# Optimization experiments

Hardware: AMD Instinct MI355X
Metric: run time of the kernel (lower is better)

The kernel has to match this reference:

```python
import jax, jax.numpy as jnp
import numpy as np


def setup_inputs() -> dict:
    key = jax.random.key(0)
    kA, kB = jax.random.split(key)
    N = 8192
    A = jax.random.normal(kA, (N, N), dtype=jnp.float32)
    B = jax.random.normal(kB, (N, N), dtype=jnp.float32)
    return {"A": A, "B": B}


def reference(A, B):
    # Kernel computes C[i,j] = sum_{k=i..j} A[i,k] * B[k,j] for i <= j, 0 elsewhere.
    # This equals triu(triu(A) @ triu(B)): k>=i is enforced by triu(A),
    # k<=j by triu(B), and output restricted to the upper triangle.
    C = jnp.triu(A) @ jnp.triu(B)
    return jnp.triu(C)
```

## Files before the change

kernel.cpp:

```cpp
#include <hip/hip_runtime.h>
#include <hip/hip_bf16.h>
#include <stdint.h>

static constexpr int ND = 8192;

typedef __attribute__((ext_vector_type(8))) short bf16x8;
typedef __attribute__((ext_vector_type(4))) float f32x4;

#define GLOBAL_AS __attribute__((address_space(1)))
#define LDS_AS __attribute__((address_space(3)))

__device__ __forceinline__ void gld_lds16(const void* g, void* l) {
    __builtin_amdgcn_global_load_lds((const GLOBAL_AS void*)g, (LDS_AS void*)l, 16, 0, 0);
}

__device__ __forceinline__ unsigned short f2bf(float x) {
    union { float f; uint32_t u; } v; v.f = x;
    uint32_t u = v.u;
    uint32_t r = (u + 0x7fffu + ((u >> 16) & 1u)) >> 16;
    return (unsigned short)r;
}

__global__ void conv_a(const float* __restrict__ A, unsigned short* __restrict__ Aw) {
    uint32_t g = blockIdx.x * 256u + threadIdx.x;
    int i  = (int)(g >> 10);
    int k0 = (int)(g & 1023u) << 3;
    if (k0 + 8 <= (i & ~255)) return;
    const float* src = A + (size_t)i * ND + k0;
    float4 lo = *(const float4*)src;
    float4 hi = *(const float4*)(src + 4);
    float vals[8] = {lo.x, lo.y, lo.z, lo.w, hi.x, hi.y, hi.z, hi.w};
    unsigned short out[8];
#pragma unroll
    for (int e = 0; e < 8; ++e) {
        int k = k0 + e;
        out[e] = (k >= i) ? f2bf(vals[e]) : (unsigned short)0;
    }
    *(uint4*)(Aw + (size_t)i * ND + k0) = *(const uint4*)out;
}

__global__ void conv_bt(const float* __restrict__ B, unsigned short* __restrict__ Bt) {
    __shared__ float tile[64][65];
    int tk = blockIdx.x, tj = blockIdx.y;
    int t = threadIdx.x;
    int k0 = tk * 64, j0 = tj * 64;

    if (k0 > j0 + 63) {
        if (tk >= ((tj >> 2) + 1) * 4) return;
        int jl = t >> 4;
        int kl = (t & 15) * 4;
#pragma unroll
        for (int r = 0; r < 4; ++r) {
            int j = j0 + jl + r * 16;
            *(uint2*)(Bt + (size_t)j * ND + k0 + kl) = make_uint2(0u, 0u);
        }
        return;
    }
    {
        int kl  = t >> 4;
        int jl4 = (t & 15) * 4;
#pragma unroll
        for (int r = 0; r < 4; ++r) {
            int k = k0 + kl + r * 16;
            float4 v = *(const float4*)(B + (size_t)k * ND + j0 + jl4);
            tile[kl + r * 16][jl4 + 0] = v.x;
            tile[kl + r * 16][jl4 + 1] = v.y;
            tile[kl + r * 16][jl4 + 2] = v.z;
            tile[kl + r * 16][jl4 + 3] = v.w;
        }
    }
    __syncthreads();
    {
        int jl  = t >> 4;
        int kl4 = (t & 15) * 4;
#pragma unroll
        for (int r = 0; r < 4; ++r) {
            int j = j0 + jl + r * 16;
            unsigned short o[4];
#pragma unroll
            for (int e = 0; e < 4; ++e) {
                int k = k0 + kl4 + e;
                float v = tile[kl4 + e][jl + r * 16];
                o[e] = (k <= j) ? f2bf(v) : (unsigned short)0;
            }
            *(uint2*)(Bt + (size_t)j * ND + k0 + kl4) = *(const uint2*)o;
        }
    }
}

__global__ __launch_bounds__(256) void zero_lower(float* __restrict__ C) {
    int bid = blockIdx.x;
    int ti = (int)((1.0f + sqrtf(8.0f * (float)bid + 1.0f)) * 0.5f);
    while (ti * (ti + 1) / 2 <= bid) ++ti;
    while (ti * (ti - 1) / 2 > bid) --ti;
    int tj = bid - ti * (ti - 1) / 2;
    if ((ti >> 1) == (tj >> 1)) return;
    int t = threadIdx.x;
    float* base = C + (size_t)(ti * 128) * ND + tj * 128;
    float4 z = {0.f, 0.f, 0.f, 0.f};
#pragma unroll
    for (int it = 0; it < 16; ++it) {
        int row = it * 8 + (t >> 5);
        *(float4*)(base + (size_t)row * ND + (t & 31) * 4) = z;
    }
}

__global__ __launch_bounds__(256) void zero_split(float* __restrict__ C) {
    int bid = blockIdx.x;
    int tile = bid >> 2, quad = bid & 3;
    int d = 31, rem = tile;
    while (rem >= 32 - d) { rem -= 32 - d; --d; }
    int tib = rem, tjb = tib + d;
    int t = threadIdx.x;
    float* base = C + (size_t)(tib * 256 + (quad >> 1) * 128) * ND
                    + tjb * 256 + (quad & 1) * 128;
    float4 z = {0.f, 0.f, 0.f, 0.f};
#pragma unroll
    for (int it = 0; it < 16; ++it) {
        int row = it * 8 + (t >> 5);
        *(float4*)(base + (size_t)row * ND + (t & 31) * 4) = z;
    }
}

#define BAR() __builtin_amdgcn_s_barrier()
#define WAIT_LGKM0() asm volatile("s_waitcnt lgkmcnt(0)" ::: "memory")
#define WAIT_VM4() asm volatile("s_waitcnt vmcnt(4)" ::: "memory")
#define WAIT_VM0() asm volatile("s_waitcnt vmcnt(0)" ::: "memory")
#define PRIO(x) __builtin_amdgcn_s_setprio(x)

#define LDA(BUF, MH) do { \
    _Pragma("unroll") for (int m_ = 0; m_ < 4; ++m_) \
    _Pragma("unroll") for (int kk_ = 0; kk_ < 2; ++kk_) \
        a_frag[m_][kk_] = *(const bf16x8*)(lds0 + (((BUF)*2 + 0)*2 + (MH))*8192 \
            + (a_lr + m_*16)*64 + (((kk_*4 + khi) ^ lanelo) << 3)); \
} while (0)

#define LDB(BUF, NH) do { \
    _Pragma("unroll") for (int n_ = 0; n_ < 2; ++n_) \
    _Pragma("unroll") for (int kk_ = 0; kk_ < 2; ++kk_) \
        b_frag[NH][n_][kk_] = *(const bf16x8*)(lds0 + (((BUF)*2 + 1)*2 + (NH))*8192 \
            + (b_lr + n_*16)*64 + (((kk_*4 + khi) ^ lanelo) << 3)); \
} while (0)

#define MM(MH, NH) do { \
    _Pragma("unroll") for (int kk_ = 0; kk_ < 2; ++kk_) \
    _Pragma("unroll") for (int m_ = 0; m_ < 4; ++m_) \
    _Pragma("unroll") for (int n_ = 0; n_ < 2; ++n_) \
        acc[(MH)*4 + m_][(NH)*2 + n_] = __builtin_amdgcn_mfma_f32_16x16x32_bf16( \
            a_frag[m_][kk_], b_frag[NH][n_][kk_], acc[(MH)*4 + m_][(NH)*2 + n_], 0, 0, 0); \
} while (0)

__device__ __forceinline__ void job_map(int bid, int& tib, int& tjb, int& kt0,
                                        int& nktj, bool& atom) {
    int rem = bid;
    for (int v = 64; v >= 4; --v) {
        if ((v & 1) == 0) {
            int d = (v >> 1) - 1;
            if (d >= 16) {
                int cnt = 2 * (32 - d);
                if (rem < cnt) {
                    tib = rem >> 1; tjb = tib + d;
                    nktj = v; kt0 = (rem & 1) * v; atom = true;
                    return;
                }
                rem -= cnt;
            }
        }
        if ((v & 3) == 0) {
            int d = (v >> 2) - 1;
            if (d <= 15) {
                int cnt = 32 - d;
                if (rem < cnt) {
                    tib = rem; tjb = tib + d;
                    nktj = v; kt0 = 0; atom = false;
                    return;
                }
                rem -= cnt;
            }
        }
    }
    tib = 0; tjb = 0; kt0 = 0; nktj = 4; atom = false;
}

__global__ __launch_bounds__(512, 2) void gemm_tri8(const unsigned short* __restrict__ Aw,
                                                    const unsigned short* __restrict__ Bt,
                                                    float* __restrict__ C) {
    int tib, tjb, kt0j, nkt;
    bool atom;
    job_map(blockIdx.x, tib, tjb, kt0j, nkt, atom);

    __shared__ __align__(16) unsigned short lds[2][2][2][128][64];
    unsigned short* lds0 = &lds[0][0][0][0][0];

    int t = threadIdx.x;
    int lane = t & 63, w = t >> 6;
    int wr = w >> 2, wc = w & 3;
    int lanelo = lane & 7, khi = lane >> 4;
    int a_lr = wr * 64 + (lane & 15);
    int b_lr = wc * 32 + (lane & 15);

    int kstart = tib * 256 + kt0j * 64;
    int nit = nkt >> 1;

    int srow = w * 8 + (lane >> 3);
    int sg = ((lane & 7) ^ (lane >> 3)) * 8;
    const unsigned short* gA = Aw + (size_t)(tib * 256 + srow) * ND + sg;
    const unsigned short* gB = Bt + (size_t)(tjb * 256 + srow) * ND + sg;
    unsigned short* sdst = lds0 + (w * 512 + lane * 8);

    auto STAGE = [&](int ab, int buf, int h, int ktg) {
        const unsigned short* g = (ab ? gB : gA) + (size_t)(h * 128) * ND + (kstart + ktg * 64);
        unsigned short* l = sdst + ((buf * 2 + ab) * 2 + h) * 8192;
        gld_lds16(g, l);
        gld_lds16(g + (size_t)64 * ND, l + 4096);
    };

    f32x4 acc[8][4];
#pragma unroll
    for (int m = 0; m < 8; ++m)
#pragma unroll
        for (int n = 0; n < 4; ++n) acc[m][n] = (f32x4){0.f, 0.f, 0.f, 0.f};

    bf16x8 a_frag[4][2];
    bf16x8 b_frag[2][2][2];

    STAGE(0, 0, 0, 0); STAGE(1, 0, 0, 0); STAGE(0, 0, 1, 0); STAGE(1, 0, 1, 0);
    STAGE(0, 1, 0, 1); STAGE(1, 1, 0, 1);
    WAIT_VM4();
    BAR();

    for (int I = 0; I < nit; ++I) {
        int k1 = 2 * I + 1, k2 = 2 * I + 2, k3 = 2 * I + 3;
        bool s23 = (k2 < nkt);

        LDA(0, 0); LDB(0, 0);
        STAGE(0, 1, 1, k1);
        BAR(); WAIT_LGKM0(); PRIO(1); MM(0, 0); PRIO(0); BAR();
        LDB(0, 1);
        STAGE(1, 1, 1, k1);
        BAR(); WAIT_LGKM0(); PRIO(1); MM(0, 1); PRIO(0); BAR();
        LDA(0, 1);
        if (s23) STAGE(0, 0, 0, k2);
        BAR(); WAIT_LGKM0(); PRIO(1); MM(1, 0); PRIO(0); BAR();
        if (s23) STAGE(1, 0, 0, k2);
        BAR(); PRIO(1); MM(1, 1); PRIO(0);
        if (s23) { WAIT_VM4(); } else { WAIT_VM0(); }
        BAR();
        LDA(1, 0); LDB(1, 0);
        if (s23) STAGE(0, 0, 1, k2);
        BAR(); WAIT_LGKM0(); PRIO(1); MM(0, 0); PRIO(0); BAR();
        LDB(1, 1);
        if (s23) STAGE(1, 0, 1, k2);
        BAR(); WAIT_LGKM0(); PRIO(1); MM(0, 1); PRIO(0); BAR();
        LDA(1, 1);
        if (s23) STAGE(0, 1, 0, k3);
        BAR(); WAIT_LGKM0(); PRIO(1); MM(1, 0); PRIO(0); BAR();
        if (s23) STAGE(1, 1, 0, k3);
        BAR(); PRIO(1); MM(1, 1); PRIO(0); WAIT_VM4(); BAR();
    }

#pragma unroll
    for (int mh = 0; mh < 2; ++mh)
#pragma unroll
        for (int m = 0; m < 4; ++m)
#pragma unroll
            for (int nh = 0; nh < 2; ++nh)
#pragma unroll
                for (int n = 0; n < 2; ++n) {
                    f32x4 v = acc[mh * 4 + m][nh * 2 + n];
                    int row0 = tib * 256 + mh * 128 + wr * 64 + m * 16 + (lane >> 4) * 4;
                    int col  = tjb * 256 + nh * 128 + wc * 32 + n * 16 + (lane & 15);
                    if (atom) {
#pragma unroll
                        for (int e = 0; e < 4; ++e)
                            atomicAdd(&C[(size_t)(row0 + e) * ND + col], v[e]);
                    } else {
#pragma unroll
                        for (int e = 0; e < 4; ++e)
                            C[(size_t)(row0 + e) * ND + col] = v[e];
                    }
                }
}

__global__ void tri_naive(const float* __restrict__ A, const float* __restrict__ B,
                          float* __restrict__ C) {
    int j = blockIdx.x * 64 + (threadIdx.x & 63);
    int i = blockIdx.y * 4 + (threadIdx.x >> 6);
    float s = 0.f;
    if (j >= i) {
        for (int k = i; k <= j; ++k) s += A[(size_t)i * ND + k] * B[(size_t)k * ND + j];
        C[(size_t)i * ND + j] = s;
    } else {
        C[(size_t)i * ND + j] = 0.f;
    }
}

extern "C" void kernel_launch(void* const* d_in, const int* in_sizes, int n_in,
                              void* d_out, int out_size, void* d_ws, size_t ws_size,
                              hipStream_t stream) {
    (void)in_sizes; (void)n_in; (void)out_size;
    const float* A = (const float*)d_in[0];
    const float* B = (const float*)d_in[1];
    float* C = (float*)d_out;

    const size_t halfws = (size_t)ND * ND * sizeof(unsigned short);
    if (ws_size >= 2 * halfws) {
        unsigned short* Aw = (unsigned short*)d_ws;
        unsigned short* Bt = (unsigned short*)((char*)d_ws + halfws);

        conv_a<<<dim3(ND * (ND / 8) / 256), dim3(256), 0, stream>>>(A, Aw);
        conv_bt<<<dim3(ND / 64, ND / 64), dim3(256), 0, stream>>>(B, Bt);
        zero_lower<<<dim3(2016), dim3(256), 0, stream>>>(C);
        zero_split<<<dim3(544), dim3(256), 0, stream>>>(C);
        gemm_tri8<<<dim3(664), dim3(512), 0, stream>>>(Aw, Bt, C);
    } else {
        tri_naive<<<dim3(ND / 64, ND / 4), dim3(256), 0, stream>>>(A, B, C);
    }
}
```

Baseline: 361.8 us.

## Group triangular GEMM jobs by output column per XCD for L2 reuse

Replaces the diagonal-ordered job mapping with a table that gives each XCD (bid & 7) a set of output tile columns. Blocks on the same XCD then work on the same column and share its B tiles in that XCD's L2, and the table balances total work across XCDs. The grid grows to 680 so it divides evenly into 8, and the padding blocks exit early. Because blocks now run column by column instead of in large-job-first order, the tail may be less balanced.

```diff
diff --git a/kernel.cpp b/kernel.cpp
--- a/kernel.cpp
+++ b/kernel.cpp
@@ -150,36 +150,38 @@
             a_frag[m_][kk_], b_frag[NH][n_][kk_], acc[(MH)*4 + m_][(NH)*2 + n_], 0, 0, 0); \
 } while (0)
 
-__device__ __forceinline__ void job_map(int bid, int& tib, int& tjb, int& kt0,
-                                        int& nktj, bool& atom) {
-    int rem = bid;
-    for (int v = 64; v >= 4; --v) {
-        if ((v & 1) == 0) {
-            int d = (v >> 1) - 1;
-            if (d >= 16) {
-                int cnt = 2 * (32 - d);
-                if (rem < cnt) {
-                    tib = rem >> 1; tjb = tib + d;
-                    nktj = v; kt0 = (rem & 1) * v; atom = true;
-                    return;
-                }
-                rem -= cnt;
+__device__ __forceinline__ bool job_map(int bid, int& tib, int& tjb, int& kt0,
+                                        int& nkt, bool& atom) {
+    static const int cols[8][5] = {
+        {31, 16,  8,  4,  0}, {30, 17,  9,  6, -1},
+        {29, 18, 10,  7, -1}, {28, 19, 11,  5, -1},
+        {27, 20, 12,  3,  1}, {26, 21, 13,  2, -1},
+        {25, 22, 14, -1, -1}, {24, 23, 15, -1, -1}};
+    int xcd = bid & 7, slot = bid >> 3;
+#pragma unroll
+    for (int c = 0; c < 5; ++c) {
+        int tj = cols[xcd][c];
+        if (tj < 0) return false;
+        int nsp = (tj - 15 > 0) ? (tj - 15) : 0;
+        int n = (tj + 1) + nsp;
+        if (slot < n) {
+            tjb = tj;
+            if (slot < 2 * nsp) {
+                tib = slot >> 1;
+                nkt = 2 * (tj - tib + 1);
+                kt0 = (slot & 1) * nkt;
+                atom = true;
+            } else {
+                tib = nsp + (slot - 2 * nsp);
+                nkt = 4 * (tj - tib + 1);
+                kt0 = 0;
+                atom = false;
             }
+            return true;
         }
-        if ((v & 3) == 0) {
-            int d = (v >> 2) - 1;
-            if (d <= 15) {
-                int cnt = 32 - d;
-                if (rem < cnt) {
-                    tib = rem; tjb = tib + d;
-                    nktj = v; kt0 = 0; atom = false;
-                    return;
-                }
-                rem -= cnt;
-            }
-        }
-    }
-    tib = 0; tjb = 0; kt0 = 0; nktj = 4; atom = false;
+        slot -= n;
+    }
+    return false;
 }
 
 __global__ __launch_bounds__(512, 2) void gemm_tri8(const unsigned short* __restrict__ Aw,
@@ -187,7 +189,7 @@
                                                     float* __restrict__ C) {
     int tib, tjb, kt0j, nkt;
     bool atom;
-    job_map(blockIdx.x, tib, tjb, kt0j, nkt, atom);
+    if (!job_map(blockIdx.x, tib, tjb, kt0j, nkt, atom)) return;
 
     __shared__ __align__(16) unsigned short lds[2][2][2][128][64];
     unsigned short* lds0 = &lds[0][0][0][0][0];
@@ -312,7 +314,7 @@
         conv_bt<<<dim3(ND / 64, ND / 64), dim3(256), 0, stream>>>(B, Bt);
         zero_lower<<<dim3(2016), dim3(256), 0, stream>>>(C);
         zero_split<<<dim3(544), dim3(256), 0, stream>>>(C);
-        gemm_tri8<<<dim3(664), dim3(512), 0, stream>>>(Aw, Bt, C);
+        gemm_tri8<<<dim3(680), dim3(512), 0, stream>>>(Aw, Bt, C);
     } else {
         tri_naive<<<dim3(ND / 64, ND / 4), dim3(256), 0, stream>>>(A, B, C);
     }
```

Measured after the change: 372.1 us. +2.9%, slower.
